# Optimization experiments

Hardware: AMD Instinct MI355X
Metric: run time of the kernel (lower is better)

## Reference

```python
import jax, jax.numpy as jnp
import numpy as np

B, L, D = 2, 2048, 2048
H, KVH, HD, FD = 8, 1, 256, 64   # heads, kv heads, head_dim, feature_dim
CHUNK = 64


def setup_inputs() -> dict:
    key = jax.random.key(0)
    ks = jax.random.split(key, 8)
    hidden_states = jax.random.normal(ks[0], (B, L, D), dtype=jnp.float32)
    # Gemma-style RoPE tables over half the head dim
    half = HD // 2
    inv_freq = 1.0 / (10000.0 ** (jnp.arange(half, dtype=jnp.float32) / half))
    ang = jnp.arange(L, dtype=jnp.float32)[:, None] * inv_freq[None, :]  # [L, half]
    freqs_cos, freqs_sin = jnp.cos(ang), jnp.sin(ang)
    mask = jnp.ones((1, 1, L, L), dtype=bool)  # unused in linear path
    s = 0.02
    Wq = jax.random.normal(ks[1], (D, H * HD), dtype=jnp.float32) * s
    Wk = jax.random.normal(ks[2], (D, KVH * HD), dtype=jnp.float32) * s
    Wv = jax.random.normal(ks[3], (D, KVH * HD), dtype=jnp.float32) * s
    Wo = jax.random.normal(ks[4], (H * HD, D), dtype=jnp.float32) * s
    fmq = jax.random.normal(ks[5], (H, HD, FD), dtype=jnp.float32) * s
    fmk = jax.random.normal(ks[6], (H, HD, FD), dtype=jnp.float32) * s
    return dict(hidden_states=hidden_states, freqs_cos=freqs_cos, freqs_sin=freqs_sin,
                mask=mask, Wq=Wq, Wk=Wk, Wv=Wv, Wo=Wo, fmq=fmq, fmk=fmk)


def _rope(x, cos, sin):
    # x: [B, L, h, HD]; Gemma complex RoPE: first half = real, second half = imag
    half = x.shape[-1] // 2
    x1, x2 = x[..., :half], x[..., half:]
    c = cos[None, :, None, :]
    s = sin[None, :, None, :]
    return jnp.concatenate([x1 * c - x2 * s, x1 * s + x2 * c], axis=-1)


def _hedgehog(x, W):
    # x: [B, H, L, HD], W: [H, HD, FD] -> softmax over cat([xW, -xW]) -> [B,H,L,2*FD]
    p = jnp.einsum('bhld,hdf->bhlf', x, W)
    return jax.nn.softmax(jnp.concatenate([p, -p], axis=-1), axis=-1)


def _chunk_linear_attn(q, k, v, chunk=CHUNK):
    # q,k: [B,H,L,F]; v: [B,H,L,HD]; chunked causal linear attention
    b, h, l, f = q.shape
    dv = v.shape[-1]
    n = l // chunk
    q = q.reshape(b, h, n, chunk, f) * (f ** -0.5)
    k = k.reshape(b, h, n, chunk, f)
    v = v.reshape(b, h, n, chunk, dv)
    kv = jnp.einsum('bhncf,bhncd->bhnfd', k, v)            # per-chunk KV
    kv = jnp.cumsum(kv, axis=2)
    kv = jnp.concatenate([jnp.zeros_like(kv[:, :, :1]), kv[:, :, :-1]], axis=2)  # exclusive prefix
    inter = jnp.einsum('bhncf,bhnfd->bhncd', q, kv)        # cross-chunk term
    s = jnp.einsum('bhnif,bhnjf->bhnij', q, k)             # intra-chunk scores
    tri = jnp.tril(jnp.ones((chunk, chunk), dtype=bool))
    s = jnp.where(tri, s, 0.0)
    intra = jnp.einsum('bhnij,bhnjd->bhnid', s, v)
    return (inter + intra).reshape(b, h, l, dv)


def reference(hidden_states, freqs_cos, freqs_sin, mask, Wq, Wk, Wv, Wo, fmq, fmk):
    b, l, _ = hidden_states.shape
    q = (hidden_states @ Wq).reshape(b, l, H, HD)
    k = (hidden_states @ Wk).reshape(b, l, KVH, HD)
    v = (hidden_states @ Wv).reshape(b, l, KVH, HD)
    q = _rope(q, freqs_cos, freqs_sin)
    k = _rope(k, freqs_cos, freqs_sin)
    # repeat_interleave kv heads to num_heads (MQA expansion)
    rep = H // KVH
    k = jnp.repeat(k, rep, axis=2)
    v = jnp.repeat(v, rep, axis=2)
    q = jnp.transpose(q, (0, 2, 1, 3))  # [B,H,L,HD]
    k = jnp.transpose(k, (0, 2, 1, 3))
    v = jnp.transpose(v, (0, 2, 1, 3))
    q = _hedgehog(q, fmq)
    k = _hedgehog(k, fmk)
    o = _chunk_linear_attn(q, k, v)                         # [B,H,L,HD]
    o = jnp.transpose(o, (0, 2, 1, 3)).reshape(b, l, H * HD)
    return o @ Wo
```

## Files before the change

kernel.cpp:

```cpp
#include <hip/hip_runtime.h>

#define B_ 2
#define L_ 2048
#define D_ 2048
#define H_ 8
#define HD_ 256
#define FD_ 64
#define F_ 128
#define NC_ 32
#define M_ (B_*L_)
#define SCALE_Q 0.08838834764831845f

typedef unsigned short u16;
typedef __attribute__((ext_vector_type(8))) short bf16x8;
typedef __attribute__((ext_vector_type(8))) unsigned short u16x8;
typedef __attribute__((ext_vector_type(16))) float f32x16;

#define FMA4(a_, s_, v_) { (a_).x += (s_)*(v_).x; (a_).y += (s_)*(v_).y; \
                           (a_).z += (s_)*(v_).z; (a_).w += (s_)*(v_).w; }


__device__ __forceinline__ u16 bf16_rne(float x) {
  unsigned u = __float_as_uint(x);
  return (u16)((u + 0x7fffu + ((u >> 16) & 1u)) >> 16);
}
__device__ __forceinline__ void bf16_split(float x, u16& h, u16& l) {
  unsigned u = __float_as_uint(x);
  unsigned hb = (u + 0x7fffu + ((u >> 16) & 1u)) >> 16;
  h = (u16)hb;
  float hf = __uint_as_float(hb << 16);
  l = bf16_rne(x - hf);
}

__device__ __forceinline__ void gl_lds16(const u16* g, u16* l) {
  __builtin_amdgcn_global_load_lds(
      (const __attribute__((address_space(1))) unsigned int*)g,
      (__attribute__((address_space(3))) unsigned int*)l, 16, 0, 0);
}

__device__ __forceinline__ void wtrans_body(const float* __restrict__ W, int Nsrc,
                                            int n0, u16* __restrict__ dst,
                                            int P, int kt) {
  int t = threadIdx.x;
  int nn = t & 127, kh = t >> 7;
  const float* src = W + (size_t)(kt * 32 + kh * 16) * Nsrc + n0 + nn;
  u16x8 u0, u1;
  #pragma unroll
  for (int kk = 0; kk < 8; ++kk) u0[kk] = bf16_rne(src[(size_t)kk * Nsrc]);
  #pragma unroll
  for (int kk = 0; kk < 8; ++kk) u1[kk] = bf16_rne(src[(size_t)(kk + 8) * Nsrc]);
  size_t base = ((size_t)P * 64 + kt) * 4096 + (size_t)((nn >> 6) & 1) * 2048
              + (size_t)kh * 1024 + (size_t)((nn >> 5) & 1) * 512
              + (size_t)(nn & 31) * 8;
  *(u16x8*)(dst + base) = u0;
  *(u16x8*)(dst + base + 256) = u1;
}

__global__ __launch_bounds__(256)
void prep_kernel(const float* __restrict__ hs,
                 const float* __restrict__ Wq, const float* __restrict__ Wk,
                 const float* __restrict__ Wv,
                 u16* __restrict__ hsHt, u16* __restrict__ hsLt,
                 u16* __restrict__ WTh) {
  int bid = blockIdx.x;
  if (bid < 4096) {
    int gid = bid * 256 + threadIdx.x;
    int r = gid >> 8, u = gid & 255;
    const float* src = hs + (size_t)r * 2048 + u * 8;
    float4 v0 = *(const float4*)src, v1 = *(const float4*)(src + 4);
    float vals[8] = {v0.x, v0.y, v0.z, v0.w, v1.x, v1.y, v1.z, v1.w};
    u16x8 hv, lv;
    #pragma unroll
    for (int j = 0; j < 8; ++j) { u16 hh, ll; bf16_split(vals[j], hh, ll); hv[j] = hh; lv[j] = ll; }
    size_t off = ((size_t)(r >> 6) * 64 + (u >> 2)) * 2048
               + (size_t)((u >> 1) & 1) * 1024 + (size_t)((r >> 5) & 1) * 512
               + (size_t)(u & 1) * 256 + (size_t)(r & 31) * 8;
    *(u16x8*)(hsHt + off) = hv;
    *(u16x8*)(hsLt + off) = lv;
  } else {
    int idx = bid - 4096;
    int P = idx >> 6, kt = idx & 63;
    const float* W; int Nsrc, n0;
    if (P < 16)      { W = Wq; Nsrc = 2048; n0 = P * 128; }
    else if (P < 18) { W = Wk; Nsrc = 256;  n0 = (P - 16) * 128; }
    else             { W = Wv; Nsrc = 256;  n0 = (P - 18) * 128; }
    wtrans_body(W, Nsrc, n0, WTh, P, kt);
  }
}

__global__ __launch_bounds__(256)
void wtrans_wo(const float* __restrict__ Wo, u16* __restrict__ WoTh) {
  wtrans_body(Wo, 2048, blockIdx.x * 128, WoTh, blockIdx.x, blockIdx.y);
}

__device__ __forceinline__ void mfma_body(
    const u16* __restrict__ AtH, const u16* __restrict__ AtL,
    const u16* __restrict__ Bt, float* __restrict__ C, int cstride,
    int bm, int bn) {
  __shared__ __align__(16) u16 AsH[2048];
  __shared__ __align__(16) u16 AsL[2048];
  __shared__ __align__(16) u16 Bs[4096];
  const int t = threadIdx.x, lane = t & 63, wv = t >> 6;
  const u16* aSrc = (wv ? AtL : AtH) + (size_t)bm * 131072 + lane * 8;
  const u16* bSrc = Bt + (size_t)bn * 262144 + wv * 2048 + lane * 8;
  u16* aDst = wv ? AsL : AsH;
  u16* bDst = Bs + wv * 2048;

  f32x16 acc[2][2];
  #pragma unroll
  for (int a = 0; a < 2; ++a)
    #pragma unroll
    for (int b2 = 0; b2 < 2; ++b2)
      #pragma unroll
      for (int r = 0; r < 16; ++r) acc[a][b2][r] = 0.f;

  for (int kt = 0; kt < 64; ++kt) {
    const u16* ak = aSrc + (size_t)kt * 2048;
    const u16* bk = bSrc + (size_t)kt * 4096;
    __syncthreads();
    #pragma unroll
    for (int c = 0; c < 4; ++c) {
      gl_lds16(ak + c * 512, aDst + c * 512);
      gl_lds16(bk + c * 512, bDst + c * 512);
    }
    __syncthreads();

    #pragma unroll
    for (int ks = 0; ks < 2; ++ks) {
      const u16* ph = AsH + ks * 1024 + lane * 8;
      const u16* pl = AsL + ks * 1024 + lane * 8;
      const u16* pb = Bs + wv * 2048 + ks * 1024 + lane * 8;
      bf16x8 a0 = *(const bf16x8*)ph;
      bf16x8 a1 = *(const bf16x8*)(ph + 512);
      bf16x8 b0 = *(const bf16x8*)pb;
      bf16x8 b1 = *(const bf16x8*)(pb + 512);
      acc[0][0] = __builtin_amdgcn_mfma_f32_32x32x16_bf16(a0, b0, acc[0][0], 0, 0, 0);
      acc[0][1] = __builtin_amdgcn_mfma_f32_32x32x16_bf16(a0, b1, acc[0][1], 0, 0, 0);
      acc[1][0] = __builtin_amdgcn_mfma_f32_32x32x16_bf16(a1, b0, acc[1][0], 0, 0, 0);
      acc[1][1] = __builtin_amdgcn_mfma_f32_32x32x16_bf16(a1, b1, acc[1][1], 0, 0, 0);
      bf16x8 l0 = *(const bf16x8*)pl;
      bf16x8 l1 = *(const bf16x8*)(pl + 512);
      acc[0][0] = __builtin_amdgcn_mfma_f32_32x32x16_bf16(l0, b0, acc[0][0], 0, 0, 0);
      acc[0][1] = __builtin_amdgcn_mfma_f32_32x32x16_bf16(l0, b1, acc[0][1], 0, 0, 0);
      acc[1][0] = __builtin_amdgcn_mfma_f32_32x32x16_bf16(l1, b0, acc[1][0], 0, 0, 0);
      acc[1][1] = __builtin_amdgcn_mfma_f32_32x32x16_bf16(l1, b1, acc[1][1], 0, 0, 0);
    }
  }

  const int fr = lane & 31, g = lane >> 5;
  float* Cp = C + (size_t)(bm * 64) * cstride + wv * 64;
  #pragma unroll
  for (int mt = 0; mt < 2; ++mt)
    #pragma unroll
    for (int nt = 0; nt < 2; ++nt) {
      #pragma unroll
      for (int r = 0; r < 16; ++r) {
        int row = mt * 32 + (r & 3) + 8 * (r >> 2) + 4 * g;
        Cp[(size_t)row * cstride + nt * 32 + fr] = acc[mt][nt][r];
      }
    }
}

__global__ __launch_bounds__(128, 4)
void mfma_qkv(const u16* __restrict__ hsHt, const u16* __restrict__ hsLt,
              const u16* __restrict__ WTh,
              float* __restrict__ q, float* __restrict__ k, float* __restrict__ v) {
  int bn = blockIdx.x, bm = blockIdx.y;
  float* Cb; int cs, co;
  if (bn < 16)      { Cb = q; cs = 2048; co = bn * 128; }
  else if (bn < 18) { Cb = k; cs = 256;  co = (bn - 16) * 128; }
  else              { Cb = v; cs = 256;  co = (bn - 18) * 128; }
  mfma_body(hsHt, hsLt, WTh, Cb + co, cs, bm, bn);
}

__global__ __launch_bounds__(128, 4)
void mfma_wo(const u16* __restrict__ oHt, const u16* __restrict__ oLt,
             const u16* __restrict__ WoTh, float* __restrict__ out) {
  mfma_body(oHt, oLt, WoTh, out + blockIdx.x * 128, 2048, blockIdx.y, blockIdx.x);
}

__device__ __forceinline__ float wave_max64(float v) {
  #pragma unroll
  for (int off = 32; off > 0; off >>= 1) v = fmaxf(v, __shfl_xor(v, off, 64));
  return v;
}
__device__ __forceinline__ float wave_sum64(float v) {
  #pragma unroll
  for (int off = 32; off > 0; off >>= 1) v += __shfl_xor(v, off, 64);
  return v;
}

__global__ __launch_bounds__(256)
void hedgehog_kernel(const float* __restrict__ q, const float* __restrict__ kx,
                     const float* __restrict__ fmq, const float* __restrict__ fmk,
                     const float* __restrict__ cosb, const float* __restrict__ sinb,
                     float* __restrict__ qf, float* __restrict__ kf) {
  __shared__ __align__(16) float rows[4][4][256];
  int bid = blockIdx.x;
  const float* x; const float* fm; float* out; int nh_in, gb;
  if (bid < 2048) { x = q;  fm = fmq; out = qf; nh_in = 8; gb = bid * 4; }
  else            { x = kx; fm = fmk; out = kf; nh_in = 1; gb = (bid - 2048) * 4; }
  int wave = threadIdx.x >> 6, lane = threadIdx.x & 63;
  int g = gb + wave;
  int l4 = g & (L_/4 - 1);
  int bh = g / (L_/4);
  int h = bh & 7, b = bh >> 3;
  int l0 = l4 * 4;
  size_t rstride = (nh_in == 1) ? (size_t)HD_ : (size_t)H_ * HD_;
  const float* xrow = (nh_in == 1)
      ? x + (size_t)(b * L_ + l0) * HD_
      : x + ((size_t)(b * L_ + l0) * H_ + h) * HD_;
  int dd = (lane & 31) * 4;
  #pragma unroll
  for (int r = 0; r < 4; ++r) {
    float4 v = *(const float4*)(xrow + r * rstride + lane * 4);
    float4 u;
    u.x = __shfl_xor(v.x, 32, 64); u.y = __shfl_xor(v.y, 32, 64);
    u.z = __shfl_xor(v.z, 32, 64); u.w = __shfl_xor(v.w, 32, 64);
    int l = l0 + r;
    float4 c = *(const float4*)(cosb + (size_t)l * 128 + dd);
    float4 s = *(const float4*)(sinb + (size_t)l * 128 + dd);
    float4 ro;
    if (lane < 32) {
      ro.x = v.x * c.x - u.x * s.x; ro.y = v.y * c.y - u.y * s.y;
      ro.z = v.z * c.z - u.z * s.z; ro.w = v.w * c.w - u.w * s.w;
    } else {
      ro.x = u.x * s.x + v.x * c.x; ro.y = u.y * s.y + v.y * c.y;
      ro.z = u.z * s.z + v.z * c.z; ro.w = u.w * s.w + v.w * c.w;
    }
    *(float4*)&rows[wave][r][lane * 4] = ro;
  }
  __syncthreads();

  const float* fmh = fm + (size_t)h * HD_ * FD_;
  float p0 = 0.f, p1 = 0.f, p2 = 0.f, p3 = 0.f;
  for (int d2 = 0; d2 < HD_; d2 += 4) {
    float w0 = fmh[(d2 + 0) * FD_ + lane];
    float w1 = fmh[(d2 + 1) * FD_ + lane];
    float w2 = fmh[(d2 + 2) * FD_ + lane];
    float w3 = fmh[(d2 + 3) * FD_ + lane];
    float4 r0 = *(const float4*)&rows[wave][0][d2];
    float4 r1 = *(const float4*)&rows[wave][1][d2];
    float4 r2 = *(const float4*)&rows[wave][2][d2];
    float4 r3 = *(const float4*)&rows[wave][3][d2];
    p0 += r0.x * w0 + r0.y * w1 + r0.z * w2 + r0.w * w3;
    p1 += r1.x * w0 + r1.y * w1 + r1.z * w2 + r1.w * w3;
    p2 += r2.x * w0 + r2.y * w1 + r2.z * w2 + r2.w * w3;
    p3 += r3.x * w0 + r3.y * w1 + r3.z * w2 + r3.w * w3;
  }
  float p[4] = {p0, p1, p2, p3};
  #pragma unroll
  for (int r = 0; r < 4; ++r) {
    float m = wave_max64(fabsf(p[r]));
    float e1 = __expf(p[r] - m);
    float e2 = __expf(-p[r] - m);
    float z = wave_sum64(e1 + e2);
    float inv = 1.0f / z;
    size_t base = ((size_t)bh * L_ + l0 + r) * F_;
    out[base + lane]      = e1 * inv;
    out[base + 64 + lane] = e2 * inv;
  }
}

__global__ __launch_bounds__(256)
void chunk_kv_kernel(const float* __restrict__ kf, const float* __restrict__ v,
                     float* __restrict__ kvc) {
  __shared__ __align__(16) float kfs[64][128];
  int n = blockIdx.x & (NC_ - 1), bh = blockIdx.x >> 5;
  int b = bh >> 3;
  const float* kfp = kf + ((size_t)bh * L_ + (size_t)n * 64) * F_;
  int t = threadIdx.x;
  #pragma unroll
  for (int it = 0; it < 8; ++it) {
    int flat = t * 4 + it * 1024;
    *(float4*)&kfs[flat >> 7][flat & 127] = *(const float4*)(kfp + flat);
  }
  __syncthreads();
  int dg = t & 63;
  int fg = t >> 6;
  const float* vp = v + (size_t)(b * L_ + n * 64) * HD_ + dg * 4;
  float* outp = kvc + (size_t)blockIdx.x * (F_ * HD_) + dg * 4;
  #pragma unroll
  for (int pass = 0; pass < 4; ++pass) {
    int f0 = fg * 8 + pass * 32;
    float4 acc[8];
    #pragma unroll
    for (int i = 0; i < 8; ++i) acc[i] = make_float4(0.f, 0.f, 0.f, 0.f);
    for (int j = 0; j < 64; ++j) {
      float4 vv = *(const float4*)(vp + (size_t)j * HD_);
      float4 ka = *(const float4*)&kfs[j][f0];
      float4 kb = *(const float4*)&kfs[j][f0 + 4];
      FMA4(acc[0], ka.x, vv); FMA4(acc[1], ka.y, vv);
      FMA4(acc[2], ka.z, vv); FMA4(acc[3], ka.w, vv);
      FMA4(acc[4], kb.x, vv); FMA4(acc[5], kb.y, vv);
      FMA4(acc[6], kb.z, vv); FMA4(acc[7], kb.w, vv);
    }
    #pragma unroll
    for (int ff = 0; ff < 8; ++ff)
      *(float4*)(outp + (size_t)(f0 + ff) * HD_) = acc[ff];
  }
}

__global__ __launch_bounds__(256)
void chunk_scan_kernel(float* __restrict__ kvc) {
  size_t gid = ((size_t)blockIdx.x * 256 + threadIdx.x) * 4;
  size_t bh = gid >> 15;
  size_t fd = gid & 32767;
  float* p = kvc + bh * ((size_t)NC_ * F_ * HD_) + fd;
  float4 run = make_float4(0.f, 0.f, 0.f, 0.f);
  #pragma unroll
  for (int n = 0; n < NC_; ++n) {
    float4 val = *(float4*)(p + (size_t)n * (F_ * HD_));
    *(float4*)(p + (size_t)n * (F_ * HD_)) = run;
    run.x += val.x; run.y += val.y; run.z += val.z; run.w += val.w;
  }
}

__global__ __launch_bounds__(256)
void chunk_attn_kernel(const float* __restrict__ qf, const float* __restrict__ kf,
                       const float* __restrict__ v, const float* __restrict__ kvc,
                       u16* __restrict__ oHt, u16* __restrict__ oLt) {
  __shared__ __align__(16) float qsT[128][68];
  __shared__ __align__(16) float ksS[128][68];
  float (*ssT)[68] = (float(*)[68])ksS;
  int n = blockIdx.x & (NC_ - 1), bh = blockIdx.x >> 5;
  int h = bh & 7, b = bh >> 3;
  int t = threadIdx.x;
  const float* qp = qf + ((size_t)bh * L_ + (size_t)n * 64) * F_;
  const float* kp = kf + ((size_t)bh * L_ + (size_t)n * 64) * F_;
  #pragma unroll
  for (int it = 0; it < 8; ++it) {
    int flat = t * 4 + it * 1024;
    int j = flat >> 7, f = flat & 127;
    float4 qv = *(const float4*)(qp + flat);
    qsT[f + 0][j] = qv.x * SCALE_Q; qsT[f + 1][j] = qv.y * SCALE_Q;
    qsT[f + 2][j] = qv.z * SCALE_Q; qsT[f + 3][j] = qv.w * SCALE_Q;
    float4 kv_ = *(const float4*)(kp + flat);
    ksS[f + 0][j] = kv_.x; ksS[f + 1][j] = kv_.y;
    ksS[f + 2][j] = kv_.z; ksS[f + 3][j] = kv_.w;
  }
  __syncthreads();

  float4 accs[4];
  {
    int j4 = (t & 15) * 4, i4 = (t >> 4) * 4;
    #pragma unroll
    for (int i = 0; i < 4; ++i) accs[i] = make_float4(0.f, 0.f, 0.f, 0.f);
    for (int f = 0; f < F_; ++f) {
      float4 a4 = *(const float4*)&qsT[f][i4];
      float4 b4 = *(const float4*)&ksS[f][j4];
      FMA4(accs[0], a4.x, b4); FMA4(accs[1], a4.y, b4);
      FMA4(accs[2], a4.z, b4); FMA4(accs[3], a4.w, b4);
    }
  }
  __syncthreads();
  {
    int j4 = (t & 15) * 4, i4 = (t >> 4) * 4;
    #pragma unroll
    for (int ii = 0; ii < 4; ++ii) {
      float sv[4] = {accs[ii].x, accs[ii].y, accs[ii].z, accs[ii].w};
      #pragma unroll
      for (int jj = 0; jj < 4; ++jj) {
        int i = i4 + ii, j = j4 + jj;
        ssT[j][i] = (j <= i) ? sv[jj] : 0.f;
      }
    }
  }
  __syncthreads();

  int dgrp = t & 31, rs = t >> 5;
  int d0 = dgrp * 8;
  int i0 = rs * 8;
  const float* kvp = kvc + (size_t)blockIdx.x * (F_ * HD_) + d0;
  const float* vp = v + (size_t)(b * L_ + n * 64) * HD_ + d0;
  float4 acc[8][2];
  #pragma unroll
  for (int i = 0; i < 8; ++i) {
    acc[i][0] = make_float4(0.f, 0.f, 0.f, 0.f);
    acc[i][1] = make_float4(0.f, 0.f, 0.f, 0.f);
  }
  for (int f = 0; f < F_; ++f) {
    float4 kv0 = *(const float4*)(kvp + (size_t)f * HD_);
    float4 kv1 = *(const float4*)(kvp + (size_t)f * HD_ + 4);
    float4 a0 = *(const float4*)&qsT[f][i0];
    float4 a1 = *(const float4*)&qsT[f][i0 + 4];
    FMA4(acc[0][0], a0.x, kv0); FMA4(acc[0][1], a0.x, kv1);
    FMA4(acc[1][0], a0.y, kv0); FMA4(acc[1][1], a0.y, kv1);
    FMA4(acc[2][0], a0.z, kv0); FMA4(acc[2][1], a0.z, kv1);
    FMA4(acc[3][0], a0.w, kv0); FMA4(acc[3][1], a0.w, kv1);
    FMA4(acc[4][0], a1.x, kv0); FMA4(acc[4][1], a1.x, kv1);
    FMA4(acc[5][0], a1.y, kv0); FMA4(acc[5][1], a1.y, kv1);
    FMA4(acc[6][0], a1.z, kv0); FMA4(acc[6][1], a1.z, kv1);
    FMA4(acc[7][0], a1.w, kv0); FMA4(acc[7][1], a1.w, kv1);
  }
  for (int j = 0; j < 64; ++j) {
    float4 v0 = *(const float4*)(vp + (size_t)j * HD_);
    float4 v1 = *(const float4*)(vp + (size_t)j * HD_ + 4);
    float4 s0 = *(const float4*)&ssT[j][i0];
    float4 s1 = *(const float4*)&ssT[j][i0 + 4];
    FMA4(acc[0][0], s0.x, v0); FMA4(acc[0][1], s0.x, v1);
    FMA4(acc[1][0], s0.y, v0); FMA4(acc[1][1], s0.y, v1);
    FMA4(acc[2][0], s0.z, v0); FMA4(acc[2][1], s0.z, v1);
    FMA4(acc[3][0], s0.w, v0); FMA4(acc[3][1], s0.w, v1);
    FMA4(acc[4][0], s1.x, v0); FMA4(acc[4][1], s1.x, v1);
    FMA4(acc[5][0], s1.y, v0); FMA4(acc[5][1], s1.y, v1);
    FMA4(acc[6][0], s1.z, v0); FMA4(acc[6][1], s1.z, v1);
    FMA4(acc[7][0], s1.w, v0); FMA4(acc[7][1], s1.w, v1);
  }
  int p = (b * L_ + n * 64) >> 6;
  size_t obase = ((size_t)p * 64 + h * 8 + (dgrp >> 2)) * 2048
               + (size_t)((dgrp >> 1) & 1) * 1024 + (size_t)(dgrp & 1) * 256;
  #pragma unroll
  for (int ii = 0; ii < 8; ++ii) {
    int i = i0 + ii;
    size_t off = obase + (size_t)((i >> 5) & 1) * 512 + (size_t)(i & 31) * 8;
    float vals[8] = {acc[ii][0].x, acc[ii][0].y, acc[ii][0].z, acc[ii][0].w,
                     acc[ii][1].x, acc[ii][1].y, acc[ii][1].z, acc[ii][1].w};
    u16x8 hv, lv;
    #pragma unroll
    for (int jj = 0; jj < 8; ++jj) { u16 hh, ll; bf16_split(vals[jj], hh, ll); hv[jj] = hh; lv[jj] = ll; }
    *(u16x8*)(oHt + off) = hv;
    *(u16x8*)(oLt + off) = lv;
  }
}

extern "C" void kernel_launch(void* const* d_in, const int* in_sizes, int n_in,
                              void* d_out, int out_size, void* d_ws, size_t ws_size,
                              hipStream_t stream) {
  const float* hs   = (const float*)d_in[0];
  const float* fcos = (const float*)d_in[1];
  const float* fsin = (const float*)d_in[2];
  const float* Wq  = (const float*)d_in[4];
  const float* Wk  = (const float*)d_in[5];
  const float* Wv  = (const float*)d_in[6];
  const float* Wo  = (const float*)d_in[7];
  const float* fmq = (const float*)d_in[8];
  const float* fmk = (const float*)d_in[9];
  float* out = (float*)d_out;

  float* ws = (float*)d_ws;
  float* q  = ws;
  float* k  = q  + (size_t)M_ * 2048;
  float* v  = k  + (size_t)M_ * 256;
  float* qf = v  + (size_t)M_ * 256;
  float* kf = qf + (size_t)B_ * H_ * L_ * F_;
  float* kv = kf + (size_t)B_ * H_ * L_ * F_;

  u16* hsHt = (u16*)kv;
  u16* hsLt = hsHt + (size_t)M_ * 2048;
  u16* WTh  = hsLt + (size_t)M_ * 2048;
  u16* WoTh = (u16*)kv;
  u16* oHt  = (u16*)q;
  u16* oLt  = oHt + (size_t)M_ * 2048;

  prep_kernel<<<4096 + 1280, 256, 0, stream>>>(hs, Wq, Wk, Wv, hsHt, hsLt, WTh);
  mfma_qkv<<<dim3(20, 64), 128, 0, stream>>>(hsHt, hsLt, WTh, q, k, v);
  hedgehog_kernel<<<2048 + 2048, 256, 0, stream>>>(q, k, fmq, fmk, fcos, fsin, qf, kf);
  chunk_kv_kernel<<<B_ * H_ * NC_, 256, 0, stream>>>(kf, v, kv);
  chunk_scan_kernel<<<(B_ * H_ * F_ * HD_) / 1024, 256, 0, stream>>>(kv);
  chunk_attn_kernel<<<B_ * H_ * NC_, 256, 0, stream>>>(qf, kf, v, kv, oHt, oLt);
  wtrans_wo<<<dim3(16, 64), 256, 0, stream>>>(Wo, WoTh);
  mfma_wo<<<dim3(16, 64), 128, 0, stream>>>(oHt, oLt, WoTh, out);
}
```

Baseline: 526.4 us.

## Use larger 256x128 MFMA tiles with triple-buffered LDS for Q and Wo GEMMs

Adds a new GEMM body in which 8 waves cooperatively compute a 256x128 output tile, with a three-stage LDS ring fed by direct global-to-LDS loads. Each loaded B tile is reused across four times as many rows, and prefetching runs two k-steps ahead. The Q projection and Wo projection now use this body, while K/V stay on the old small-tile kernel in a separate launch. In exchange there are fewer blocks (256 per GEMM), which may leave some CUs idle, plus higher LDS use per block and an extra kernel launch.

```diff
diff --git a/kernel.cpp b/kernel.cpp
--- a/kernel.cpp
+++ b/kernel.cpp
@@ -161,22 +161,128 @@
     }
 }
 
+#define SUB_ 20480
+
+__device__ __forceinline__ void mfma_big_body(
+    const u16* __restrict__ AtH, const u16* __restrict__ AtL,
+    const u16* __restrict__ Bt, float* __restrict__ C, int cstride,
+    int bm, int bn) {
+  __shared__ __align__(16) u16 lds[3 * SUB_];
+  const int t = threadIdx.x, lane = t & 63, wv = t >> 6;
+  const int wm = wv >> 1, wn = wv & 1;
+
+  const u16* gs[5];
+  unsigned lo[5], gst[5];
+  #pragma unroll
+  for (int j = 0; j < 5; ++j) {
+    int line = wv * 5 + j;
+    if (line < 16) {
+      gs[j] = AtH + ((size_t)(4 * bm + (line >> 2)) * 64) * 2048
+                  + (size_t)(line & 3) * 512 + lane * 8;
+      lo[j] = line * 512; gst[j] = 2048;
+    } else if (line < 32) {
+      int l2 = line - 16;
+      gs[j] = AtL + ((size_t)(4 * bm + (l2 >> 2)) * 64) * 2048
+                  + (size_t)(l2 & 3) * 512 + lane * 8;
+      lo[j] = 8192 + l2 * 512; gst[j] = 2048;
+    } else {
+      int l3 = line - 32;
+      gs[j] = Bt + (size_t)bn * 262144 + (size_t)l3 * 512 + lane * 8;
+      lo[j] = 16384 + l3 * 512; gst[j] = 4096;
+    }
+  }
+
+  f32x16 acc[2][2];
+  #pragma unroll
+  for (int a = 0; a < 2; ++a)
+    #pragma unroll
+    for (int b2 = 0; b2 < 2; ++b2)
+      #pragma unroll
+      for (int r = 0; r < 16; ++r) acc[a][b2][r] = 0.f;
+
+  auto stage = [&](int kt_, int boff_) {
+    #pragma unroll
+    for (int j = 0; j < 5; ++j)
+      gl_lds16(gs[j] + (size_t)kt_ * gst[j], lds + boff_ + lo[j]);
+  };
+
+  stage(0, 0);
+  stage(1, SUB_);
+  asm volatile("s_waitcnt vmcnt(5)" ::: "memory");
+  __builtin_amdgcn_s_barrier();
+  __builtin_amdgcn_sched_barrier(0);
+
+  int cb = 0;
+  for (int kt = 0; kt < 64; ++kt) {
+    int sb = cb + 2 * SUB_; if (sb >= 3 * SUB_) sb -= 3 * SUB_;
+    if (kt < 62) stage(kt + 2, sb);
+    const u16* base = lds + cb;
+    #pragma unroll
+    for (int ks = 0; ks < 2; ++ks) {
+      const u16* ph = base + wm * 2048 + ks * 1024 + lane * 8;
+      const u16* pb = base + 16384 + wn * 2048 + ks * 1024 + lane * 8;
+      bf16x8 a0 = *(const bf16x8*)ph;
+      bf16x8 a1 = *(const bf16x8*)(ph + 512);
+      bf16x8 l0 = *(const bf16x8*)(ph + 8192);
+      bf16x8 l1 = *(const bf16x8*)(ph + 8704);
+      bf16x8 b0 = *(const bf16x8*)pb;
+      bf16x8 b1 = *(const bf16x8*)(pb + 512);
+      __builtin_amdgcn_s_setprio(1);
+      acc[0][0] = __builtin_amdgcn_mfma_f32_32x32x16_bf16(a0, b0, acc[0][0], 0, 0, 0);
+      acc[0][1] = __builtin_amdgcn_mfma_f32_32x32x16_bf16(a0, b1, acc[0][1], 0, 0, 0);
+      acc[1][0] = __builtin_amdgcn_mfma_f32_32x32x16_bf16(a1, b0, acc[1][0], 0, 0, 0);
+      acc[1][1] = __builtin_amdgcn_mfma_f32_32x32x16_bf16(a1, b1, acc[1][1], 0, 0, 0);
+      acc[0][0] = __builtin_amdgcn_mfma_f32_32x32x16_bf16(l0, b0, acc[0][0], 0, 0, 0);
+      acc[0][1] = __builtin_amdgcn_mfma_f32_32x32x16_bf16(l0, b1, acc[0][1], 0, 0, 0);
+      acc[1][0] = __builtin_amdgcn_mfma_f32_32x32x16_bf16(l1, b0, acc[1][0], 0, 0, 0);
+      acc[1][1] = __builtin_amdgcn_mfma_f32_32x32x16_bf16(l1, b1, acc[1][1], 0, 0, 0);
+      __builtin_amdgcn_s_setprio(0);
+    }
+    asm volatile("s_waitcnt lgkmcnt(0)" ::: "memory");
+    if (kt < 62) asm volatile("s_waitcnt vmcnt(5)" ::: "memory");
+    else         asm volatile("s_waitcnt vmcnt(0)" ::: "memory");
+    __builtin_amdgcn_s_barrier();
+    __builtin_amdgcn_sched_barrier(0);
+    cb += SUB_; if (cb == 3 * SUB_) cb = 0;
+  }
+
+  const int fr = lane & 31, g = lane >> 5;
+  float* Cp = C + (size_t)(bm * 256 + wm * 64) * cstride + wn * 64;
+  #pragma unroll
+  for (int mt = 0; mt < 2; ++mt)
+    #pragma unroll
+    for (int nt = 0; nt < 2; ++nt) {
+      #pragma unroll
+      for (int r = 0; r < 16; ++r) {
+        int row = mt * 32 + (r & 3) + 8 * (r >> 2) + 4 * g;
+        Cp[(size_t)row * cstride + nt * 32 + fr] = acc[mt][nt][r];
+      }
+    }
+}
+
+__global__ __launch_bounds__(512, 2)
+void mfma_q(const u16* __restrict__ hsHt, const u16* __restrict__ hsLt,
+            const u16* __restrict__ WTh, float* __restrict__ q) {
+  mfma_big_body(hsHt, hsLt, WTh, q + blockIdx.x * 128, 2048,
+                blockIdx.y, blockIdx.x);
+}
+
 __global__ __launch_bounds__(128, 4)
-void mfma_qkv(const u16* __restrict__ hsHt, const u16* __restrict__ hsLt,
-              const u16* __restrict__ WTh,
-              float* __restrict__ q, float* __restrict__ k, float* __restrict__ v) {
-  int bn = blockIdx.x, bm = blockIdx.y;
-  float* Cb; int cs, co;
-  if (bn < 16)      { Cb = q; cs = 2048; co = bn * 128; }
-  else if (bn < 18) { Cb = k; cs = 256;  co = (bn - 16) * 128; }
-  else              { Cb = v; cs = 256;  co = (bn - 18) * 128; }
-  mfma_body(hsHt, hsLt, WTh, Cb + co, cs, bm, bn);
-}
-
-__global__ __launch_bounds__(128, 4)
+void mfma_kv(const u16* __restrict__ hsHt, const u16* __restrict__ hsLt,
+             const u16* __restrict__ WTh,
+             float* __restrict__ k, float* __restrict__ v) {
+  int bn = blockIdx.x;
+  float* Cb; int co;
+  if (bn < 2) { Cb = k; co = bn * 128; }
+  else        { Cb = v; co = (bn - 2) * 128; }
+  mfma_body(hsHt, hsLt, WTh, Cb + co, 256, blockIdx.y, 16 + bn);
+}
+
+__global__ __launch_bounds__(512, 2)
 void mfma_wo(const u16* __restrict__ oHt, const u16* __restrict__ oLt,
              const u16* __restrict__ WoTh, float* __restrict__ out) {
-  mfma_body(oHt, oLt, WoTh, out + blockIdx.x * 128, 2048, blockIdx.y, blockIdx.x);
+  mfma_big_body(oHt, oLt, WoTh, out + blockIdx.x * 128, 2048,
+                blockIdx.y, blockIdx.x);
 }
 
 __device__ __forceinline__ float wave_max64(float v) {
@@ -454,11 +560,12 @@
   u16* oLt  = oHt + (size_t)M_ * 2048;
 
   prep_kernel<<<4096 + 1280, 256, 0, stream>>>(hs, Wq, Wk, Wv, hsHt, hsLt, WTh);
-  mfma_qkv<<<dim3(20, 64), 128, 0, stream>>>(hsHt, hsLt, WTh, q, k, v);
+  mfma_q<<<dim3(16, 16), 512, 0, stream>>>(hsHt, hsLt, WTh, q);
+  mfma_kv<<<dim3(4, 64), 128, 0, stream>>>(hsHt, hsLt, WTh, k, v);
   hedgehog_kernel<<<2048 + 2048, 256, 0, stream>>>(q, k, fmq, fmk, fcos, fsin, qf, kf);
   chunk_kv_kernel<<<B_ * H_ * NC_, 256, 0, stream>>>(kf, v, kv);
   chunk_scan_kernel<<<(B_ * H_ * F_ * HD_) / 1024, 256, 0, stream>>>(kv);
   chunk_attn_kernel<<<B_ * H_ * NC_, 256, 0, stream>>>(qf, kf, v, kv, oHt, oLt);
   wtrans_wo<<<dim3(16, 64), 256, 0, stream>>>(Wo, WoTh);
-  mfma_wo<<<dim3(16, 64), 128, 0, stream>>>(oHt, oLt, WoTh, out);
-}
+  mfma_wo<<<dim3(16, 16), 512, 0, stream>>>(oHt, oLt, WoTh, out);
+}
```

Measured after the change: 538.9 us. 2.4% more time.
